# Optimization experiments

Measured on AMD Instinct MI355X. Metric: run time of the kernel, lower is better.

Reference implementation:

```python
import jax, jax.numpy as jnp
import numpy as np

B, V, TG = 512, 16, 48
LAB, MED, GLU, E = 256, 192, 16, 64


def _attn_enc(x, W1, b1, Wq, Wk):
    # Attn_encoder: project then self-attend; out [..., L, H]
    h = jnp.tanh(x @ W1 + b1)
    q, k = h @ Wq, h @ Wk
    a = jax.nn.softmax(jnp.einsum('...qd,...kd->...qk', q, k) / jnp.sqrt(jnp.float32(Wq.shape[1])), axis=-1)
    return a @ h


def _mha(q, k, v, Wq, Wk, Wv, Wo, H=4):
    # module's MHA: output length follows v (v acts as query side)
    d = Wq.shape[1]; dh = d // H
    qh = (v @ Wq).reshape(v.shape[:-1] + (H, dh))
    kh = (k @ Wk).reshape(k.shape[:-1] + (H, dh))
    vh = (q @ Wv).reshape(q.shape[:-1] + (H, dh))
    a = jax.nn.softmax(jnp.einsum('...qhd,...khd->...hqk', qh, kh) / jnp.sqrt(jnp.float32(dh)), axis=-1)
    o = jnp.einsum('...hqk,...khd->...qhd', a, vh)
    return o.reshape(o.shape[:-2] + (d,)) @ Wo


def _forward(lab, glu, time, med, ehr_adj, ddi_adj, time_adj,
             Ws1, bs1, Ws2, bs2, Wl1, bl1, Wl2, bl2, Wl3, bl3,
             Wm1, bm1, Wmq, Wmk, Wg1, bg1, Wgq, Wgk,
             gru_Wx, gru_Wh, gru_b,
             m1_Wq, m1_Wk, m1_Wv, m1_Wo, m2_Wq, m2_Wk, m2_Wv, m2_Wo,
             Wo1, bo1, Wo2, bo2):
    Bn, Vn, Tn = glu.shape
    G = gru_Wh.shape[0]
    # static_ll: [B, E//2] repeated over visits
    s = jax.nn.relu(lab @ Ws1 + bs1)
    s = jax.nn.relu(s @ Ws2 + bs2)
    static_fea = jnp.broadcast_to(s[:, None, :], (Bn, Vn, s.shape[-1]))
    # glu_encoder: GRU over per-visit glucose/time readings -> [B, V, GLU]
    x = jnp.stack([glu, time], -1).reshape(Bn * Vn, Tn, 2)
    xs = jnp.swapaxes(x, 0, 1)  # [T, BV, 2]
    def step(h, xt):
        g = xt @ gru_Wx + gru_b
        gh = h @ gru_Wh
        z = jax.nn.sigmoid(g[:, :G] + gh[:, :G])
        r = jax.nn.sigmoid(g[:, G:2 * G] + gh[:, G:2 * G])
        n = jnp.tanh(g[:, 2 * G:] + r * gh[:, 2 * G:])
        return (1.0 - z) * n + z * h, None
    hT, _ = jax.lax.scan(step, jnp.zeros((Bn * Vn, G), glu.dtype), xs)
    glu_enc = hT.reshape(Bn, Vn, G)
    glu_rep = _attn_enc(glu_enc, Wg1, bg1, Wgq, Wgk)        # [B, V, E//2]
    patient_rep = jnp.concatenate([glu_rep, static_fea], -1)  # [B, V, E]
    med_rep = _attn_enc(med[:, :-1, :], Wm1, bm1, Wmq, Wmk)   # [B, V-1, E]
    # drug memory from graph adjacencies (shared across patients)
    drug_mem = (ehr_adj @ Wl1 + bl1) + (time_adj @ Wl2 + bl2) - (ddi_adj @ Wl3 + bl3)  # [MED, E]
    E_en = _mha(patient_rep, patient_rep, med_rep, m1_Wq, m1_Wk, m1_Wv, m1_Wo)  # [B, V-1, E]
    dm = jnp.broadcast_to(drug_mem, (Bn,) + drug_mem.shape)
    E_de = _mha(E_en, E_en, dm, m2_Wq, m2_Wk, m2_Wv, m2_Wo)   # [B, MED, E]
    final = E_de.reshape(Bn, -1)
    o = jax.nn.relu(final)
    o = jax.nn.relu(o @ Wo1 + bo1)
    return o @ Wo2 + bo2  # [B, MED]


def setup_inputs() -> dict:
    ks = iter(jax.random.split(jax.random.key(0), 64))
    def nrm(shape, s=0.05):
        return jax.random.normal(next(ks), shape, dtype=jnp.float32) * s
    z = lambda *shape: jnp.zeros(shape, jnp.float32)
    d = {}
    d['lab'] = jax.random.normal(next(ks), (B, LAB), dtype=jnp.float32)
    d['glu'] = jax.random.normal(next(ks), (B, V, TG), dtype=jnp.float32)
    d['time'] = jax.random.uniform(next(ks), (B, V, TG), dtype=jnp.float32)
    d['med'] = jax.random.uniform(next(ks), (B, V, MED), dtype=jnp.float32)
    d['ehr_adj'] = jax.random.uniform(next(ks), (MED, MED), dtype=jnp.float32)
    d['ddi_adj'] = jax.random.uniform(next(ks), (MED, MED), dtype=jnp.float32)
    d['time_adj'] = jax.random.uniform(next(ks), (MED, MED), dtype=jnp.float32)
    d['Ws1'] = nrm((LAB, E)); d['bs1'] = z(E)
    d['Ws2'] = nrm((E, E // 2)); d['bs2'] = z(E // 2)
    d['Wl1'] = nrm((MED, E)); d['bl1'] = z(E)
    d['Wl2'] = nrm((MED, E)); d['bl2'] = z(E)
    d['Wl3'] = nrm((MED, E)); d['bl3'] = z(E)
    d['Wm1'] = nrm((MED, E)); d['bm1'] = z(E)
    d['Wmq'] = nrm((E, E // 2)); d['Wmk'] = nrm((E, E // 2))
    d['Wg1'] = nrm((GLU, E // 2)); d['bg1'] = z(E // 2)
    d['Wgq'] = nrm((E // 2, E // 4)); d['Wgk'] = nrm((E // 2, E // 4))
    d['gru_Wx'] = nrm((2, 3 * GLU)); d['gru_Wh'] = nrm((GLU, 3 * GLU)); d['gru_b'] = z(3 * GLU)
    for p in ['m1', 'm2']:
        for w in ['Wq', 'Wk', 'Wv', 'Wo']:
            d[p + '_' + w] = nrm((E, E))
    d['Wo1'] = nrm((E * MED, E * MED // 8)); d['bo1'] = z(E * MED // 8)
    d['Wo2'] = nrm((E * MED // 8, MED)); d['bo2'] = z(MED)
    return d


def reference(lab, glu, time, med, ehr_adj, ddi_adj, time_adj,
              Ws1, bs1, Ws2, bs2, Wl1, bl1, Wl2, bl2, Wl3, bl3,
              Wm1, bm1, Wmq, Wmk, Wg1, bg1, Wgq, Wgk,
              gru_Wx, gru_Wh, gru_b,
              m1_Wq, m1_Wk, m1_Wv, m1_Wo, m2_Wq, m2_Wk, m2_Wv, m2_Wo,
              Wo1, bo1, Wo2, bo2):
    return _forward(lab, glu, time, med, ehr_adj, ddi_adj, time_adj,
                    Ws1, bs1, Ws2, bs2, Wl1, bl1, Wl2, bl2, Wl3, bl3,
                    Wm1, bm1, Wmq, Wmk, Wg1, bg1, Wgq, Wgk,
                    gru_Wx, gru_Wh, gru_b,
                    m1_Wq, m1_Wk, m1_Wv, m1_Wo, m2_Wq, m2_Wk, m2_Wv, m2_Wo,
                    Wo1, bo1, Wo2, bo2)
```

## Files before the change

kernel.cpp:

```cpp
#include <hip/hip_runtime.h>
#include <math.h>

#define DEVINL __device__ __forceinline__

DEVINL float sigm(float x) { return 1.0f / (1.0f + __expf(-x)); }
DEVINL float tanh_fast(float x) { return 2.0f / (1.0f + __expf(-2.0f * x)) - 1.0f; }
DEVINL unsigned short bf16rne(float f) {
    unsigned u = __float_as_uint(f);
    return (unsigned short)((u + 0x7FFFu + ((u >> 16) & 1u)) >> 16);
}

typedef __attribute__((ext_vector_type(8))) short bf16x8;
typedef __attribute__((ext_vector_type(4))) float f32x4;

__global__ void gemm_small(const float* __restrict__ A, const float* __restrict__ W,
                           const float* __restrict__ bias, float* __restrict__ C,
                           int M, int N, int K, int act, int vgroup)
{
    int idx = blockIdx.x * blockDim.x + threadIdx.x;
    if (idx >= M * N) return;
    int m = idx / N, n = idx - m * N;
    int am = m;
    if (vgroup) { int g = m / vgroup; am = g * (vgroup + 1) + (m - g * vgroup); }
    const float* a = A + (size_t)am * K;
    const float* w = W + n;
    float acc = bias ? bias[n] : 0.0f;
    for (int k = 0; k < K; k += 4) {
        float4 av = *(const float4*)&a[k];
        float w0 = w[(size_t)k * N];
        float w1 = w[(size_t)(k + 1) * N];
        float w2 = w[(size_t)(k + 2) * N];
        float w3 = w[(size_t)(k + 3) * N];
        acc = fmaf(av.x, w0, acc);
        acc = fmaf(av.y, w1, acc);
        acc = fmaf(av.z, w2, acc);
        acc = fmaf(av.w, w3, acc);
    }
    if (act == 1) acc = fmaxf(acc, 0.0f);
    else if (act == 2) acc = tanh_fast(acc);
    C[idx] = acc;
}

__global__ void gemm_small_dual(const float* __restrict__ A,
    const float* __restrict__ W1, const float* __restrict__ W2,
    float* __restrict__ C1, float* __restrict__ C2, int M, int N, int K)
{
    int idx = blockIdx.x * blockDim.x + threadIdx.x;
    if (idx >= M * N) return;
    int m = idx / N, n = idx - m * N;
    const float* a = A + (size_t)m * K;
    const float* w1 = W1 + n;
    const float* w2 = W2 + n;
    float acc1 = 0.0f, acc2 = 0.0f;
    for (int k = 0; k < K; k += 4) {
        float4 av = *(const float4*)&a[k];
        float p0 = w1[(size_t)k * N],       q0 = w2[(size_t)k * N];
        float p1 = w1[(size_t)(k + 1) * N], q1 = w2[(size_t)(k + 1) * N];
        float p2 = w1[(size_t)(k + 2) * N], q2 = w2[(size_t)(k + 2) * N];
        float p3 = w1[(size_t)(k + 3) * N], q3 = w2[(size_t)(k + 3) * N];
        acc1 = fmaf(av.x, p0, acc1); acc2 = fmaf(av.x, q0, acc2);
        acc1 = fmaf(av.y, p1, acc1); acc2 = fmaf(av.y, q1, acc2);
        acc1 = fmaf(av.z, p2, acc1); acc2 = fmaf(av.z, q2, acc2);
        acc1 = fmaf(av.w, p3, acc1); acc2 = fmaf(av.w, q3, acc2);
    }
    C1[idx] = acc1;
    C2[idx] = acc2;
}

__global__ __launch_bounds__(256) void gru_wave(const float* __restrict__ glu,
    const float* __restrict__ timev, const float* __restrict__ Wx,
    const float* __restrict__ Wh, const float* __restrict__ bb,
    float* __restrict__ out)
{
    __shared__ float sWh[768], sWx[96], sb[48];
    int tid = threadIdx.x;
    for (int i = tid; i < 768; i += 256) sWh[i] = Wh[i];
    if (tid < 96) sWx[tid] = Wx[tid];
    if (tid < 48) sb[tid] = bb[tid];
    __syncthreads();
    int j = tid & 15;
    int seq = blockIdx.x * 16 + (tid >> 4);
    int gbase = (tid & 63) & 0x30;
    float whz[16], whr[16], whn[16];
#pragma unroll
    for (int i = 0; i < 16; ++i) {
        whz[i] = sWh[i * 48 + j];
        whr[i] = sWh[i * 48 + 16 + j];
        whn[i] = sWh[i * 48 + 32 + j];
    }
    float wxz0 = sWx[j],      wxr0 = sWx[16 + j], wxn0 = sWx[32 + j];
    float wxz1 = sWx[48 + j], wxr1 = sWx[64 + j], wxn1 = sWx[80 + j];
    float bz = sb[j], br = sb[16 + j], bn = sb[32 + j];
    const float* gp = glu + (size_t)seq * 48;
    const float* tp = timev + (size_t)seq * 48;
    float h = 0.0f;
    for (int t = 0; t < 48; ++t) {
        float gl = gp[t], tm = tp[t];
        float gz = fmaf(gl, wxz0, fmaf(tm, wxz1, bz));
        float gr = fmaf(gl, wxr0, fmaf(tm, wxr1, br));
        float gn = fmaf(gl, wxn0, fmaf(tm, wxn1, bn));
        float ghn = 0.0f;
#pragma unroll
        for (int i = 0; i < 16; ++i) {
            float hb = __shfl(h, gbase + i, 64);
            gz = fmaf(hb, whz[i], gz);
            gr = fmaf(hb, whr[i], gr);
            ghn = fmaf(hb, whn[i], ghn);
        }
        float z = sigm(gz), r = sigm(gr);
        float n = tanh_fast(gn + r * ghn);
        h = (1.0f - z) * n + z * h;
    }
    out[(size_t)seq * 16 + j] = h;
}

__global__ __launch_bounds__(256) void glu_attn(const float* __restrict__ hg,
    const float* __restrict__ Wq, const float* __restrict__ Wk,
    const float* __restrict__ s2, float* __restrict__ patient)
{
    int b = blockIdx.x, tid = threadIdx.x;
    __shared__ float sh[512], sq[256], sk[256], ss[256];
    sh[tid] = hg[(size_t)b * 512 + tid];
    sh[256 + tid] = hg[(size_t)b * 512 + 256 + tid];
    __syncthreads();
    {
        int p = tid >> 4, j = tid & 15;
        float aq = 0.0f, ak = 0.0f;
        for (int i = 0; i < 32; ++i) {
            float hv = sh[p * 32 + i];
            aq = fmaf(hv, Wq[i * 16 + j], aq);
            ak = fmaf(hv, Wk[i * 16 + j], ak);
        }
        sq[tid] = aq; sk[tid] = ak;
    }
    __syncthreads();
    {
        int p = tid >> 4, pk = tid & 15;
        float a = 0.0f;
        for (int j = 0; j < 16; ++j) a = fmaf(sq[p * 16 + j], sk[pk * 16 + j], a);
        ss[tid] = a * 0.25f;
    }
    __syncthreads();
    if (tid < 16) {
        float mx = -1e30f;
        for (int k = 0; k < 16; ++k) mx = fmaxf(mx, ss[tid * 16 + k]);
        float sum = 0.0f;
        for (int k = 0; k < 16; ++k) { float e = __expf(ss[tid * 16 + k] - mx); ss[tid * 16 + k] = e; sum += e; }
        float inv = 1.0f / sum;
        for (int k = 0; k < 16; ++k) ss[tid * 16 + k] *= inv;
    }
    __syncthreads();
    for (int o = tid; o < 512; o += 256) {
        int p = o >> 5, c = o & 31;
        float acc = 0.0f;
        for (int pk = 0; pk < 16; ++pk) acc = fmaf(ss[p * 16 + pk], sh[pk * 32 + c], acc);
        patient[((size_t)b * 16 + p) * 64 + c] = acc;
        patient[((size_t)b * 16 + p) * 64 + 32 + c] = s2[(size_t)b * 32 + c];
    }
}

__global__ __launch_bounds__(256) void med_attn(const float* __restrict__ hm,
    const float* __restrict__ Wq, const float* __restrict__ Wk,
    float* __restrict__ med_rep)
{
    int b = blockIdx.x, tid = threadIdx.x;
    __shared__ float sh[960], sq[480], sk[480], ss[225];
    for (int i = tid; i < 960; i += 256) sh[i] = hm[(size_t)b * 960 + i];
    __syncthreads();
    for (int o = tid; o < 480; o += 256) {
        int p = o >> 5, j = o & 31;
        float aq = 0.0f, ak = 0.0f;
        for (int i = 0; i < 64; ++i) {
            float hv = sh[p * 64 + i];
            aq = fmaf(hv, Wq[i * 32 + j], aq);
            ak = fmaf(hv, Wk[i * 32 + j], ak);
        }
        sq[o] = aq; sk[o] = ak;
    }
    __syncthreads();
    if (tid < 225) {
        int p = tid / 15, pk = tid - p * 15;
        float a = 0.0f;
        for (int j = 0; j < 32; ++j) a = fmaf(sq[p * 32 + j], sk[pk * 32 + j], a);
        ss[tid] = a * 0.17677669529663687f;
    }
    __syncthreads();
    if (tid < 15) {
        float mx = -1e30f;
        for (int k = 0; k < 15; ++k) mx = fmaxf(mx, ss[tid * 15 + k]);
        float sum = 0.0f;
        for (int k = 0; k < 15; ++k) { float e = __expf(ss[tid * 15 + k] - mx); ss[tid * 15 + k] = e; sum += e; }
        float inv = 1.0f / sum;
        for (int k = 0; k < 15; ++k) ss[tid * 15 + k] *= inv;
    }
    __syncthreads();
    for (int o = tid; o < 960; o += 256) {
        int p = o >> 6, c = o & 63;
        float acc = 0.0f;
        for (int pk = 0; pk < 15; ++pk) acc = fmaf(ss[p * 15 + pk], sh[pk * 64 + c], acc);
        med_rep[(size_t)b * 960 + o] = acc;
    }
}

__global__ void drugmem_kernel(const float* __restrict__ ehr, const float* __restrict__ tadj,
    const float* __restrict__ ddi,
    const float* __restrict__ Wl1, const float* __restrict__ bl1,
    const float* __restrict__ Wl2, const float* __restrict__ bl2,
    const float* __restrict__ Wl3, const float* __restrict__ bl3,
    float* __restrict__ dm)
{
    int idx = blockIdx.x * 256 + threadIdx.x;
    if (idx >= 192 * 64) return;
    int m = idx >> 6, n = idx & 63;
    float acc = bl1[n] + bl2[n] - bl3[n];
    for (int k = 0; k < 192; ++k) {
        acc = fmaf(ehr[m * 192 + k], Wl1[k * 64 + n], acc);
        acc = fmaf(tadj[m * 192 + k], Wl2[k * 64 + n], acc);
        acc = fmaf(-ddi[m * 192 + k], Wl3[k * 64 + n], acc);
    }
    dm[idx] = acc;
}

__global__ __launch_bounds__(256) void mha1_attn(const float* __restrict__ qh1,
    const float* __restrict__ kh1, const float* __restrict__ vh1,
    const float* __restrict__ Wo, float* __restrict__ Een)
{
    int b = blockIdx.x, tid = threadIdx.x;
    __shared__ float sq[1020], sk[1088], sv[1024], ss[960], so[960];
    for (int i = tid; i < 960; i += 256) sq[(i >> 6) * 68 + (i & 63)] = qh1[(size_t)b * 960 + i];
    for (int i = tid; i < 1024; i += 256) {
        sk[(i >> 6) * 68 + (i & 63)] = kh1[(size_t)b * 1024 + i];
        sv[i] = vh1[(size_t)b * 1024 + i];
    }
    __syncthreads();
    for (int o = tid; o < 960; o += 256) {
        int hh = o / 240, rem = o - hh * 240, q = rem >> 4, k = rem & 15;
        float a = 0.0f;
        for (int d = 0; d < 16; ++d) a = fmaf(sq[q * 68 + hh * 16 + d], sk[k * 68 + hh * 16 + d], a);
        ss[o] = a * 0.25f;
    }
    __syncthreads();
    if (tid < 60) {
        int base = tid * 16;
        float mx = -1e30f;
        for (int k = 0; k < 16; ++k) mx = fmaxf(mx, ss[base + k]);
        float sum = 0.0f;
        for (int k = 0; k < 16; ++k) { float e = __expf(ss[base + k] - mx); ss[base + k] = e; sum += e; }
        float inv = 1.0f / sum;
        for (int k = 0; k < 16; ++k) ss[base + k] *= inv;
    }
    __syncthreads();
    for (int o = tid; o < 960; o += 256) {
        int q = o >> 6, j = o & 63, hh = j >> 4;
        float a = 0.0f;
        for (int k = 0; k < 16; ++k) a = fmaf(ss[hh * 240 + q * 16 + k], sv[k * 64 + j], a);
        so[o] = a;
    }
    __syncthreads();
    for (int o = tid; o < 960; o += 256) {
        int q = o >> 6, c = o & 63;
        float a = 0.0f;
        for (int j = 0; j < 64; ++j) a = fmaf(so[q * 64 + j], Wo[j * 64 + c], a);
        Een[(size_t)b * 960 + o] = a;
    }
}

__global__ __launch_bounds__(256) void mha2_attn2(const float* __restrict__ qh2,
    const float* __restrict__ kh2, const float* __restrict__ vh2,
    float* __restrict__ so_all)
{
    int b = blockIdx.x >> 2, q0 = (blockIdx.x & 3) * 48;
    int tid = threadIdx.x;
    __shared__ float skp[1020], sv[960], ss[2880];
    for (int i = tid; i < 960; i += 256) {
        skp[(i >> 6) * 68 + (i & 63)] = kh2[(size_t)b * 960 + i];
        sv[i] = vh2[(size_t)b * 960 + i];
    }
    __syncthreads();
    for (int o = tid; o < 2880; o += 256) {
        int hh = o / 720, rem = o - hh * 720, q = rem / 15, k = rem - q * 15;
        const float* qp = qh2 + (size_t)(q0 + q) * 64 + hh * 16;
        float a = 0.0f;
        for (int d = 0; d < 16; ++d) a = fmaf(qp[d], skp[k * 68 + hh * 16 + d], a);
        ss[o] = a * 0.25f;
    }
    __syncthreads();
    if (tid < 192) {
        int hh = tid / 48, q = tid - hh * 48;
        int base = hh * 720 + q * 15;
        float mx = -1e30f;
        for (int k = 0; k < 15; ++k) mx = fmaxf(mx, ss[base + k]);
        float sum = 0.0f;
        for (int k = 0; k < 15; ++k) { float e = __expf(ss[base + k] - mx); ss[base + k] = e; sum += e; }
        float inv = 1.0f / sum;
        for (int k = 0; k < 15; ++k) ss[base + k] *= inv;
    }
    __syncthreads();
    for (int o = tid; o < 3072; o += 256) {
        int q = o >> 6, j = o & 63, hh = j >> 4;
        float a = 0.0f;
        for (int k = 0; k < 15; ++k) a = fmaf(ss[hh * 720 + q * 15 + k], sv[k * 64 + j], a);
        so_all[((size_t)b * 192 + q0 + q) * 64 + j] = a;
    }
}

__global__ __launch_bounds__(256) void gemm64_relu_bf16(const float* __restrict__ A,
    const float* __restrict__ B, unsigned short* __restrict__ Obf)
{
    __shared__ float As[64 * 20];
    __shared__ float Bs[16 * 64];
    int tid = threadIdx.x;
    int m0 = blockIdx.x * 64;
    float acc[4][4] = {};
    int arow = tid >> 2, akq = (tid & 3) << 2;
    int brow = tid >> 4, bnq = (tid & 15) << 2;
    int tm0 = (tid >> 4) << 2, tn0 = (tid & 15) << 2;
    for (int kt = 0; kt < 64; kt += 16) {
        float4 av = *(const float4*)&A[(size_t)(m0 + arow) * 64 + kt + akq];
        *(float4*)&As[arow * 20 + akq] = av;
        float4 bv = *(const float4*)&B[(size_t)(kt + brow) * 64 + bnq];
        *(float4*)&Bs[brow * 64 + bnq] = bv;
        __syncthreads();
#pragma unroll
        for (int kk = 0; kk < 16; ++kk) {
            float4 b4 = *(const float4*)&Bs[kk * 64 + tn0];
            float a0 = As[(tm0 + 0) * 20 + kk];
            float a1 = As[(tm0 + 1) * 20 + kk];
            float a2 = As[(tm0 + 2) * 20 + kk];
            float a3 = As[(tm0 + 3) * 20 + kk];
            acc[0][0] = fmaf(a0, b4.x, acc[0][0]); acc[0][1] = fmaf(a0, b4.y, acc[0][1]);
            acc[0][2] = fmaf(a0, b4.z, acc[0][2]); acc[0][3] = fmaf(a0, b4.w, acc[0][3]);
            acc[1][0] = fmaf(a1, b4.x, acc[1][0]); acc[1][1] = fmaf(a1, b4.y, acc[1][1]);
            acc[1][2] = fmaf(a1, b4.z, acc[1][2]); acc[1][3] = fmaf(a1, b4.w, acc[1][3]);
            acc[2][0] = fmaf(a2, b4.x, acc[2][0]); acc[2][1] = fmaf(a2, b4.y, acc[2][1]);
            acc[2][2] = fmaf(a2, b4.z, acc[2][2]); acc[2][3] = fmaf(a2, b4.w, acc[2][3]);
            acc[3][0] = fmaf(a3, b4.x, acc[3][0]); acc[3][1] = fmaf(a3, b4.y, acc[3][1]);
            acc[3][2] = fmaf(a3, b4.z, acc[3][2]); acc[3][3] = fmaf(a3, b4.w, acc[3][3]);
        }
        __syncthreads();
    }
#pragma unroll
    for (int i = 0; i < 4; ++i) {
        unsigned r0 = (unsigned)bf16rne(fmaxf(acc[i][0], 0.f)) | ((unsigned)bf16rne(fmaxf(acc[i][1], 0.f)) << 16);
        unsigned r1 = (unsigned)bf16rne(fmaxf(acc[i][2], 0.f)) | ((unsigned)bf16rne(fmaxf(acc[i][3], 0.f)) << 16);
        uint2 v = { r0, r1 };
        *(uint2*)&Obf[(size_t)(m0 + tm0 + i) * 64 + tn0] = v;
    }
}

__global__ __launch_bounds__(256) void gemm_mfma_bf16(
    const unsigned short* __restrict__ Abf, const float* __restrict__ B,
    float* __restrict__ Cp, int M, int N, int K, int klen)
{
    __shared__ unsigned short As[128 * 64];
    __shared__ unsigned short Bs[64 * 64];
    int tid = threadIdx.x;
    int lane = tid & 63, w = tid >> 6;
    int n0 = blockIdx.x * 64, m0 = blockIdx.y * 128;
    int kbase0 = blockIdx.z * klen;
    f32x4 acc[2][4] = {};

    int bn = tid & 63, bkc = (tid >> 6) * 16;
    for (int kt = 0; kt < klen; kt += 64) {
        int kb = kbase0 + kt;
#pragma unroll
        for (int c = 0; c < 4; ++c) {
            int ch = tid + c * 256;
            int row = ch >> 3, kc0 = (ch & 7) << 3;
            uint4 v = *(const uint4*)&Abf[(size_t)(m0 + row) * K + kb + kc0];
            int bo = ((row << 7) + (kc0 << 1)) ^ ((row & 7) << 4);
            *(uint4*)((char*)As + bo) = v;
        }
        {
            const float* bp = &B[(size_t)(kb + bkc) * N + n0 + bn];
#pragma unroll
            for (int j = 0; j < 16; j += 2) {
                float f0 = bp[(size_t)j * N];
                float f1 = bp[(size_t)(j + 1) * N];
                unsigned u = (unsigned)bf16rne(f0) | ((unsigned)bf16rne(f1) << 16);
                int k = bkc + j;
                int bo = ((bn << 7) + (k << 1)) ^ ((bn & 7) << 4);
                *(unsigned*)((char*)Bs + bo) = u;
            }
        }
        __syncthreads();
#pragma unroll
        for (int kk = 0; kk < 64; kk += 32) {
            int kb2 = (kk + ((lane >> 4) << 3)) << 1;
            bf16x8 af[2], bfg[4];
#pragma unroll
            for (int fm = 0; fm < 2; ++fm) {
                int row = (w << 5) + (fm << 4) + (lane & 15);
                af[fm] = *(const bf16x8*)((const char*)As + (((row << 7) + kb2) ^ ((row & 7) << 4)));
            }
#pragma unroll
            for (int fn = 0; fn < 4; ++fn) {
                int col = (fn << 4) + (lane & 15);
                bfg[fn] = *(const bf16x8*)((const char*)Bs + (((col << 7) + kb2) ^ ((col & 7) << 4)));
            }
#pragma unroll
            for (int fm = 0; fm < 2; ++fm)
#pragma unroll
                for (int fn = 0; fn < 4; ++fn)
                    acc[fm][fn] = __builtin_amdgcn_mfma_f32_16x16x32_bf16(af[fm], bfg[fn], acc[fm][fn], 0, 0, 0);
        }
        __syncthreads();
    }
    float* cp = Cp + (size_t)blockIdx.z * M * N;
#pragma unroll
    for (int fm = 0; fm < 2; ++fm)
#pragma unroll
        for (int fn = 0; fn < 4; ++fn) {
            int row = m0 + (w << 5) + (fm << 4) + ((lane >> 4) << 2);
            int col = n0 + (fn << 4) + (lane & 15);
#pragma unroll
            for (int r = 0; r < 4; ++r)
                cp[(size_t)(row + r) * N + col] = acc[fm][fn][r];
        }
}

template <int RELU_A>
__global__ __launch_bounds__(256) void gemm_sk(const float* __restrict__ A,
    const float* __restrict__ B, float* __restrict__ Cp,
    int M, int N, int K, int klen)
{
    __shared__ float As[64 * 20];
    __shared__ float Bs[16 * 64];
    int tid = threadIdx.x;
    int n0 = blockIdx.x * 64, m0 = blockIdx.y * 64;
    int bs = blockIdx.z;
    int kbase0 = bs * klen;
    float acc[4][4] = {};
    int arow = tid >> 2, akq = (tid & 3) << 2;
    int brow = tid >> 4, bnq = (tid & 15) << 2;
    int tm0 = (tid >> 4) << 2, tn0 = (tid & 15) << 2;
    for (int kt = 0; kt < klen; kt += 16) {
        int kb = kbase0 + kt;
        float4 av = *(const float4*)&A[(size_t)(m0 + arow) * K + kb + akq];
        if (RELU_A) {
            av.x = fmaxf(av.x, 0.0f); av.y = fmaxf(av.y, 0.0f);
            av.z = fmaxf(av.z, 0.0f); av.w = fmaxf(av.w, 0.0f);
        }
        *(float4*)&As[arow * 20 + akq] = av;
        float4 bv = *(const float4*)&B[(size_t)(kb + brow) * N + n0 + bnq];
        *(float4*)&Bs[brow * 64 + bnq] = bv;
        __syncthreads();
#pragma unroll
        for (int kk = 0; kk < 16; ++kk) {
            float4 b4 = *(const float4*)&Bs[kk * 64 + tn0];
            float a0 = As[(tm0 + 0) * 20 + kk];
            float a1 = As[(tm0 + 1) * 20 + kk];
            float a2 = As[(tm0 + 2) * 20 + kk];
            float a3 = As[(tm0 + 3) * 20 + kk];
            acc[0][0] = fmaf(a0, b4.x, acc[0][0]); acc[0][1] = fmaf(a0, b4.y, acc[0][1]);
            acc[0][2] = fmaf(a0, b4.z, acc[0][2]); acc[0][3] = fmaf(a0, b4.w, acc[0][3]);
            acc[1][0] = fmaf(a1, b4.x, acc[1][0]); acc[1][1] = fmaf(a1, b4.y, acc[1][1]);
            acc[1][2] = fmaf(a1, b4.z, acc[1][2]); acc[1][3] = fmaf(a1, b4.w, acc[1][3]);
            acc[2][0] = fmaf(a2, b4.x, acc[2][0]); acc[2][1] = fmaf(a2, b4.y, acc[2][1]);
            acc[2][2] = fmaf(a2, b4.z, acc[2][2]); acc[2][3] = fmaf(a2, b4.w, acc[2][3]);
            acc[3][0] = fmaf(a3, b4.x, acc[3][0]); acc[3][1] = fmaf(a3, b4.y, acc[3][1]);
            acc[3][2] = fmaf(a3, b4.z, acc[3][2]); acc[3][3] = fmaf(a3, b4.w, acc[3][3]);
        }
        __syncthreads();
    }
    float* cp = Cp + (size_t)bs * M * N;
#pragma unroll
    for (int i = 0; i < 4; ++i)
#pragma unroll
        for (int j = 0; j < 4; ++j)
            cp[(size_t)(m0 + tm0 + i) * N + n0 + tn0 + j] = acc[i][j];
}

__global__ void reduce_bias_act(const float* __restrict__ part, const float* __restrict__ bias,
                                float* __restrict__ out, int MN, int N, int S, int relu)
{
    int idx = blockIdx.x * 256 + threadIdx.x;
    if (idx >= MN) return;
    float a = bias[idx % N];
    for (int s = 0; s < S; ++s) a += part[(size_t)s * MN + idx];
    if (relu) a = fmaxf(a, 0.0f);
    out[idx] = a;
}

extern "C" void kernel_launch(void* const* d_in, const int* in_sizes, int n_in,
                              void* d_out, int out_size, void* d_ws, size_t ws_size,
                              hipStream_t stream)
{
    const float* lab    = (const float*)d_in[0];
    const float* glu    = (const float*)d_in[1];
    const float* timev  = (const float*)d_in[2];
    const float* med    = (const float*)d_in[3];
    const float* ehr    = (const float*)d_in[4];
    const float* ddi    = (const float*)d_in[5];
    const float* tadj   = (const float*)d_in[6];
    const float* Ws1    = (const float*)d_in[7];
    const float* bs1    = (const float*)d_in[8];
    const float* Ws2    = (const float*)d_in[9];
    const float* bs2    = (const float*)d_in[10];
    const float* Wl1    = (const float*)d_in[11];
    const float* bl1    = (const float*)d_in[12];
    const float* Wl2    = (const float*)d_in[13];
    const float* bl2    = (const float*)d_in[14];
    const float* Wl3    = (const float*)d_in[15];
    const float* bl3    = (const float*)d_in[16];
    const float* Wm1    = (const float*)d_in[17];
    const float* bm1    = (const float*)d_in[18];
    const float* Wmq    = (const float*)d_in[19];
    const float* Wmk    = (const float*)d_in[20];
    const float* Wg1    = (const float*)d_in[21];
    const float* bg1    = (const float*)d_in[22];
    const float* Wgq    = (const float*)d_in[23];
    const float* Wgk    = (const float*)d_in[24];
    const float* gWx    = (const float*)d_in[25];
    const float* gWh    = (const float*)d_in[26];
    const float* gb     = (const float*)d_in[27];
    const float* m1Wq   = (const float*)d_in[28];
    const float* m1Wk   = (const float*)d_in[29];
    const float* m1Wv   = (const float*)d_in[30];
    const float* m1Wo   = (const float*)d_in[31];
    const float* m2Wq   = (const float*)d_in[32];
    const float* m2Wk   = (const float*)d_in[33];
    const float* m2Wv   = (const float*)d_in[34];
    const float* m2Wo   = (const float*)d_in[35];
    const float* Wo1    = (const float*)d_in[36];
    const float* bo1    = (const float*)d_in[37];
    const float* Wo2    = (const float*)d_in[38];
    const float* bo2    = (const float*)d_in[39];

    float* W = (float*)d_ws;
    size_t off = 0;
    auto alloc = [&](size_t n) { size_t r = off; off += (n + 3) & ~(size_t)3; return r; };
    size_t o_s1      = alloc(512 * 64);
    size_t o_s2      = alloc(512 * 32);
    size_t o_gluenc  = alloc(8192 * 16);
    size_t o_hg      = alloc(8192 * 32);
    size_t o_patient = alloc(8192 * 64);
    size_t o_medh    = alloc(7680 * 64);
    size_t o_medrep  = alloc(7680 * 64);
    size_t o_dm      = alloc(192 * 64);
    size_t o_qh2s    = alloc(192 * 64);
    size_t o_qh1     = alloc(7680 * 64);
    size_t o_kh1     = alloc(8192 * 64);
    size_t o_vh1     = alloc(8192 * 64);
    size_t o_Een     = alloc(7680 * 64);
    size_t o_kh2 = o_medh;
    size_t o_vh2 = o_qh1;
    size_t o_abf = 0;
    size_t o_so      = alloc((size_t)512 * 12288);
    size_t o_h1      = alloc((size_t)512 * 1536);
    size_t o_part    = o_so;

    {
        dim3 g(1, 8, 4);
        gemm_sk<0><<<g, 256, 0, stream>>>(lab, Ws1, W + o_part, 512, 64, 256, 64);
        reduce_bias_act<<<128, 256, 0, stream>>>(W + o_part, bs1, W + o_s1, 512 * 64, 64, 4, 1);
    }
    gemm_small<<<64, 256, 0, stream>>>(W + o_s1, Ws2, bs2, W + o_s2, 512, 32, 64, 1, 0);
    gru_wave<<<512, 256, 0, stream>>>(glu, timev, gWx, gWh, gb, W + o_gluenc);
    gemm_small<<<1024, 256, 0, stream>>>(W + o_gluenc, Wg1, bg1, W + o_hg, 8192, 32, 16, 2, 0);
    glu_attn<<<512, 256, 0, stream>>>(W + o_hg, Wgq, Wgk, W + o_s2, W + o_patient);
    gemm_small<<<1920, 256, 0, stream>>>(med, Wm1, bm1, W + o_medh, 7680, 64, 192, 2, 15);
    med_attn<<<512, 256, 0, stream>>>(W + o_medh, Wmq, Wmk, W + o_medrep);
    drugmem_kernel<<<48, 256, 0, stream>>>(ehr, tadj, ddi, Wl1, bl1, Wl2, bl2, Wl3, bl3, W + o_dm);
    gemm_small<<<48, 256, 0, stream>>>(W + o_dm, m2Wq, nullptr, W + o_qh2s, 192, 64, 64, 0, 0);
    gemm_small<<<1920, 256, 0, stream>>>(W + o_medrep, m1Wq, nullptr, W + o_qh1, 7680, 64, 64, 0, 0);
    gemm_small_dual<<<2048, 256, 0, stream>>>(W + o_patient, m1Wk, m1Wv,
                                              W + o_kh1, W + o_vh1, 8192, 64, 64);
    mha1_attn<<<512, 256, 0, stream>>>(W + o_qh1, W + o_kh1, W + o_vh1, m1Wo, W + o_Een);
    gemm_small_dual<<<1920, 256, 0, stream>>>(W + o_Een, m2Wk, m2Wv,
                                              W + o_kh2, W + o_vh2, 7680, 64, 64);
    mha2_attn2<<<2048, 256, 0, stream>>>(W + o_qh2s, W + o_kh2, W + o_vh2, W + o_so);
    gemm64_relu_bf16<<<1536, 256, 0, stream>>>(W + o_so, m2Wo, (unsigned short*)(W + o_abf));
    {
        dim3 g(24, 4, 8);
        gemm_mfma_bf16<<<g, 256, 0, stream>>>((const unsigned short*)(W + o_abf), Wo1,
                                              W + o_part, 512, 1536, 12288, 1536);
        reduce_bias_act<<<3072, 256, 0, stream>>>(W + o_part, bo1, W + o_h1, 512 * 1536, 1536, 8, 1);
    }
    {
        dim3 g(3, 8, 16);
        gemm_sk<0><<<g, 256, 0, stream>>>(W + o_h1, Wo2, W + o_part, 512, 192, 1536, 96);
        reduce_bias_act<<<384, 256, 0, stream>>>(W + o_part, bo2, (float*)d_out, 512 * 192, 192, 16, 0);
    }
}
```

Before: 254.7 us.

## Shrink MFMA GEMM tile to 64x64 with 2x2 waves and vectorize B loads

The split-K bf16 MFMA GEMM for the large Wo1 projection now uses 64x64 output tiles, with the four waves arranged 2x2, instead of 128x64 tiles. The grid doubles along M. The B (fp32 weight) tile is now loaded as float4 pairs across two rows and packed into bf16, replacing strided scalar loads down columns. The smaller tile doubles the block count, which helps occupancy and load balance. The cost is reading each weight element twice as often from global memory and L2 across M blocks.

```diff
diff --git a/kernel.cpp b/kernel.cpp
--- a/kernel.cpp
+++ b/kernel.cpp
@@ -352,56 +352,65 @@
     const unsigned short* __restrict__ Abf, const float* __restrict__ B,
     float* __restrict__ Cp, int M, int N, int K, int klen)
 {
-    __shared__ unsigned short As[128 * 64];
+    __shared__ unsigned short As[64 * 64];
     __shared__ unsigned short Bs[64 * 64];
     int tid = threadIdx.x;
-    int lane = tid & 63, w = tid >> 6;
-    int n0 = blockIdx.x * 64, m0 = blockIdx.y * 128;
+    int lane = tid & 63, wid = tid >> 6;
+    int wr = wid >> 1, wc = wid & 1;
+    int n0 = blockIdx.x * 64, m0 = blockIdx.y * 64;
     int kbase0 = blockIdx.z * klen;
-    f32x4 acc[2][4] = {};
-
-    int bn = tid & 63, bkc = (tid >> 6) * 16;
+    f32x4 acc[2][2] = {};
+
     for (int kt = 0; kt < klen; kt += 64) {
         int kb = kbase0 + kt;
 #pragma unroll
-        for (int c = 0; c < 4; ++c) {
+        for (int c = 0; c < 2; ++c) {
             int ch = tid + c * 256;
             int row = ch >> 3, kc0 = (ch & 7) << 3;
             uint4 v = *(const uint4*)&Abf[(size_t)(m0 + row) * K + kb + kc0];
             int bo = ((row << 7) + (kc0 << 1)) ^ ((row & 7) << 4);
             *(uint4*)((char*)As + bo) = v;
         }
-        {
-            const float* bp = &B[(size_t)(kb + bkc) * N + n0 + bn];
-#pragma unroll
-            for (int j = 0; j < 16; j += 2) {
-                float f0 = bp[(size_t)j * N];
-                float f1 = bp[(size_t)(j + 1) * N];
-                unsigned u = (unsigned)bf16rne(f0) | ((unsigned)bf16rne(f1) << 16);
-                int k = bkc + j;
-                int bo = ((bn << 7) + (k << 1)) ^ ((bn & 7) << 4);
-                *(unsigned*)((char*)Bs + bo) = u;
-            }
+#pragma unroll
+        for (int pass = 0; pass < 2; ++pass) {
+            int task = tid + pass * 256;
+            int n4 = (task & 15) << 2;
+            int k2 = (task >> 4) << 1;
+            const float* bp = &B[(size_t)(kb + k2) * N + n0 + n4];
+            float4 r0 = *(const float4*)bp;
+            float4 r1 = *(const float4*)(bp + N);
+            unsigned u0 = (unsigned)bf16rne(r0.x) | ((unsigned)bf16rne(r1.x) << 16);
+            unsigned u1 = (unsigned)bf16rne(r0.y) | ((unsigned)bf16rne(r1.y) << 16);
+            unsigned u2 = (unsigned)bf16rne(r0.z) | ((unsigned)bf16rne(r1.z) << 16);
+            unsigned u3 = (unsigned)bf16rne(r0.w) | ((unsigned)bf16rne(r1.w) << 16);
+            int b0 = (((n4 + 0) << 7) + (k2 << 1)) ^ (((n4 + 0) & 7) << 4);
+            int b1 = (((n4 + 1) << 7) + (k2 << 1)) ^ (((n4 + 1) & 7) << 4);
+            int b2 = (((n4 + 2) << 7) + (k2 << 1)) ^ (((n4 + 2) & 7) << 4);
+            int b3 = (((n4 + 3) << 7) + (k2 << 1)) ^ (((n4 + 3) & 7) << 4);
+            *(unsigned*)((char*)Bs + b0) = u0;
+            *(unsigned*)((char*)Bs + b1) = u1;
+            *(unsigned*)((char*)Bs + b2) = u2;
+            *(unsigned*)((char*)Bs + b3) = u3;
         }
         __syncthreads();
 #pragma unroll
         for (int kk = 0; kk < 64; kk += 32) {
             int kb2 = (kk + ((lane >> 4) << 3)) << 1;
-            bf16x8 af[2], bfg[4];
+            bf16x8 af[2], bfg[2];
 #pragma unroll
             for (int fm = 0; fm < 2; ++fm) {
-                int row = (w << 5) + (fm << 4) + (lane & 15);
+                int row = (wr << 5) + (fm << 4) + (lane & 15);
                 af[fm] = *(const bf16x8*)((const char*)As + (((row << 7) + kb2) ^ ((row & 7) << 4)));
             }
 #pragma unroll
-            for (int fn = 0; fn < 4; ++fn) {
-                int col = (fn << 4) + (lane & 15);
+            for (int fn = 0; fn < 2; ++fn) {
+                int col = (wc << 5) + (fn << 4) + (lane & 15);
                 bfg[fn] = *(const bf16x8*)((const char*)Bs + (((col << 7) + kb2) ^ ((col & 7) << 4)));
             }
 #pragma unroll
             for (int fm = 0; fm < 2; ++fm)
 #pragma unroll
-                for (int fn = 0; fn < 4; ++fn)
+                for (int fn = 0; fn < 2; ++fn)
                     acc[fm][fn] = __builtin_amdgcn_mfma_f32_16x16x32_bf16(af[fm], bfg[fn], acc[fm][fn], 0, 0, 0);
         }
         __syncthreads();
@@ -410,9 +419,9 @@
 #pragma unroll
     for (int fm = 0; fm < 2; ++fm)
 #pragma unroll
-        for (int fn = 0; fn < 4; ++fn) {
-            int row = m0 + (w << 5) + (fm << 4) + ((lane >> 4) << 2);
-            int col = n0 + (fn << 4) + (lane & 15);
+        for (int fn = 0; fn < 2; ++fn) {
+            int row = m0 + (wr << 5) + (fm << 4) + ((lane >> 4) << 2);
+            int col = n0 + (wc << 5) + (fn << 4) + (lane & 15);
 #pragma unroll
             for (int r = 0; r < 4; ++r)
                 cp[(size_t)(row + r) * N + col] = acc[fm][fn][r];
@@ -572,7 +581,7 @@
     mha2_attn2<<<2048, 256, 0, stream>>>(W + o_qh2s, W + o_kh2, W + o_vh2, W + o_so);
     gemm64_relu_bf16<<<1536, 256, 0, stream>>>(W + o_so, m2Wo, (unsigned short*)(W + o_abf));
     {
-        dim3 g(24, 4, 8);
+        dim3 g(24, 8, 8);
         gemm_mfma_bf16<<<g, 256, 0, stream>>>((const unsigned short*)(W + o_abf), Wo1,
                                               W + o_part, 512, 1536, 12288, 1536);
         reduce_bias_act<<<3072, 256, 0, stream>>>(W + o_part, bo1, W + o_h1, 512 * 1536, 1536, 8, 1);
```

Measured after the change: 273.2 us. 7.3% more time.
